# Kernel tuning notes

Measured on AMD Instinct MI355X. Metric: run time of the kernel, lower is better.

Reference implementation:

```python
import jax, jax.numpy as jnp
import numpy as np

N, E, F, ED, H, G = 100000, 400000, 143, 6, 128, 4096
NL = 3   # num_layers -> NL-1 atom GATConv layers
NT = 2   # num_timesteps


def leaky(v):
    return jnp.where(v >= 0, v, 0.01 * v)  # torch default negative_slope=0.01


def gru_cell(xin, hid, Wi, Wh, bi, bh):
    # torch.nn.GRUCell, gate order r,z,n
    gi = xin @ Wi.T + bi
    gh = hid @ Wh.T + bh
    ir, iz, inn = jnp.split(gi, 3, axis=-1)
    hr, hz, hn = jnp.split(gh, 3, axis=-1)
    r = jax.nn.sigmoid(ir + hr)
    z = jax.nn.sigmoid(iz + hz)
    n = jnp.tanh(inn + r * hn)
    return (1.0 - z) * n + z * hid


def seg_softmax(a, seg, num):
    m = jax.ops.segment_max(a, seg, num_segments=num)
    m = jnp.where(jnp.isfinite(m), m, 0.0)
    e = jnp.exp(a - m[seg])
    s = jax.ops.segment_sum(e, seg, num_segments=num)
    return e / (s[seg] + 1e-16)


def afp_forward(x, edge_attr, lin1_W, lin1_b, gc_lin1_W, gc_att_l, gc_att_r,
                gc_lin2_W, gc_bias, gru0_Wi, gru0_Wh, gru0_bi, gru0_bh,
                atom_W, atom_att_src, atom_att_dst, atom_bias,
                atom_gru_Wi, atom_gru_Wh, atom_gru_bi, atom_gru_bh,
                mol_W, mol_att_src, mol_att_dst, mol_bias,
                mol_gru_Wi, mol_gru_Wh, mol_gru_bi, mol_gru_bh,
                lin2_W, lin2_b, cls_W1, cls_b1, cls_W2, cls_b2,
                edge_index, batch, num_graphs):
    src, dst = edge_index[0], edge_index[1]
    Nn = x.shape[0]
    # lin1 + leaky_relu
    x0 = leaky(x @ lin1_W.T + lin1_b)                                  # [N,H]
    # GATEConv (edge-feature gated attention)
    t = leaky(jnp.concatenate([x0[src], edge_attr], axis=-1) @ gc_lin1_W.T)  # [E,H]
    alpha = leaky(t @ gc_att_l + (x0 @ gc_att_r)[dst])                 # [E]
    alpha = seg_softmax(alpha, dst, Nn)
    x2 = x0 @ gc_lin2_W.T
    agg = jax.ops.segment_sum(x2[src] * alpha[:, None], dst, num_segments=Nn) + gc_bias
    h = jax.nn.elu(agg)
    xh = jax.nn.relu(gru_cell(h, x0, gru0_Wi, gru0_Wh, gru0_bi, gru0_bh))
    # atom GATConv layers (single head, no self loops, slope 0.01)
    for l in range(atom_W.shape[0]):
        xl = xh @ atom_W[l].T                                          # [N,H]
        a = leaky((xl @ atom_att_src[l])[src] + (xl @ atom_att_dst[l])[dst])
        a = seg_softmax(a, dst, Nn)
        agg = jax.ops.segment_sum(xl[src] * a[:, None], dst, num_segments=Nn) + atom_bias[l]
        h = jax.nn.elu(agg)
        xh = jax.nn.relu(gru_cell(h, xh, atom_gru_Wi[l], atom_gru_Wh[l], atom_gru_bi[l], atom_gru_bh[l]))
    # molecule readout: bipartite GATConv node->graph + GRU, NT timesteps
    out = jax.nn.relu(jax.ops.segment_sum(xh, batch, num_segments=num_graphs))  # [G,H]
    xm = xh @ mol_W.T
    a_src = xm @ mol_att_src                                           # [N]
    for _ in range(NT):
        om = out @ mol_W.T
        a = leaky(a_src + (om @ mol_att_dst)[batch])
        a = seg_softmax(a, batch, num_graphs)
        agg = jax.ops.segment_sum(xm * a[:, None], batch, num_segments=num_graphs) + mol_bias
        h = jax.nn.elu(agg)
        out = jax.nn.relu(gru_cell(h, out, mol_gru_Wi, mol_gru_Wh, mol_gru_bi, mol_gru_bh))
    emb = out @ lin2_W.T + lin2_b                                      # [G,H]
    y = jax.nn.relu(emb @ cls_W1.T + cls_b1) @ cls_W2.T + cls_b2       # [G,1]
    return y[:, 0]


def setup_inputs():
    key = jax.random.key(0)
    ks = iter(jax.random.split(key, 64))
    def rn(shape, s=0.08):
        return jax.random.normal(next(ks), shape, dtype=jnp.float32) * s
    return dict(
        x=jax.random.normal(next(ks), (N, F), dtype=jnp.float32),
        edge_attr=jax.random.normal(next(ks), (E, ED), dtype=jnp.float32),
        lin1_W=rn((H, F)), lin1_b=rn((H,)),
        gc_lin1_W=rn((H, H + ED)), gc_att_l=rn((H,)), gc_att_r=rn((H,)),
        gc_lin2_W=rn((H, H)), gc_bias=rn((H,)),
        gru0_Wi=rn((3 * H, H)), gru0_Wh=rn((3 * H, H)), gru0_bi=rn((3 * H,)), gru0_bh=rn((3 * H,)),
        atom_W=rn((NL - 1, H, H)), atom_att_src=rn((NL - 1, H)), atom_att_dst=rn((NL - 1, H)), atom_bias=rn((NL - 1, H)),
        atom_gru_Wi=rn((NL - 1, 3 * H, H)), atom_gru_Wh=rn((NL - 1, 3 * H, H)),
        atom_gru_bi=rn((NL - 1, 3 * H)), atom_gru_bh=rn((NL - 1, 3 * H)),
        mol_W=rn((H, H)), mol_att_src=rn((H,)), mol_att_dst=rn((H,)), mol_bias=rn((H,)),
        mol_gru_Wi=rn((3 * H, H)), mol_gru_Wh=rn((3 * H, H)), mol_gru_bi=rn((3 * H,)), mol_gru_bh=rn((3 * H,)),
        lin2_W=rn((H, H)), lin2_b=rn((H,)),
        cls_W1=rn((64, H)), cls_b1=rn((64,)), cls_W2=rn((1, 64)), cls_b2=rn((1,)),
        edge_index=jax.random.randint(next(ks), (2, E), 0, N),
        batch=jnp.sort(jax.random.randint(next(ks), (N,), 0, G)),
        num_graphs=G,
    )


def reference(x, edge_attr, lin1_W, lin1_b, gc_lin1_W, gc_att_l, gc_att_r,
              gc_lin2_W, gc_bias, gru0_Wi, gru0_Wh, gru0_bi, gru0_bh,
              atom_W, atom_att_src, atom_att_dst, atom_bias,
              atom_gru_Wi, atom_gru_Wh, atom_gru_bi, atom_gru_bh,
              mol_W, mol_att_src, mol_att_dst, mol_bias,
              mol_gru_Wi, mol_gru_Wh, mol_gru_bi, mol_gru_bh,
              lin2_W, lin2_b, cls_W1, cls_b1, cls_W2, cls_b2,
              edge_index, batch, num_graphs):
    return afp_forward(x, edge_attr, lin1_W, lin1_b, gc_lin1_W, gc_att_l, gc_att_r,
                       gc_lin2_W, gc_bias, gru0_Wi, gru0_Wh, gru0_bi, gru0_bh,
                       atom_W, atom_att_src, atom_att_dst, atom_bias,
                       atom_gru_Wi, atom_gru_Wh, atom_gru_bi, atom_gru_bh,
                       mol_W, mol_att_src, mol_att_dst, mol_bias,
                       mol_gru_Wi, mol_gru_Wh, mol_gru_bi, mol_gru_bh,
                       lin2_W, lin2_b, cls_W1, cls_b1, cls_W2, cls_b2,
                       edge_index, batch, num_graphs)
```

## Files before the change

kernel.cpp:

```cpp
#include <hip/hip_runtime.h>

#define NND 100000
#define NED 400000
#define FEAT 143
#define FEATP 160
#define EDIM 6
#define H 128
#define NG 4096
#define NBS 391

typedef __attribute__((ext_vector_type(8))) short bf8;
typedef __attribute__((ext_vector_type(4))) float f4;

__device__ __forceinline__ float b2f(unsigned short u){
  unsigned int x = ((unsigned int)u) << 16;
  return __builtin_bit_cast(float, x);
}
__device__ __forceinline__ unsigned short f2b(float f){
  unsigned int u = __builtin_bit_cast(unsigned int, f);
  u = u + 0x7fffu + ((u >> 16) & 1u);
  return (unsigned short)(u >> 16);
}
__device__ __forceinline__ float lk(float v){ return v >= 0.f ? v : 0.01f*v; }
__device__ __forceinline__ float eluf(float v){ return v > 0.f ? v : __expf(v) - 1.f; }
__device__ __forceinline__ float sgm(float v){ return 1.f/(1.f + __expf(-v)); }
__device__ __forceinline__ float wsum(float v){
  #pragma unroll
  for(int o=32;o>0;o>>=1) v += __shfl_xor(v,o);
  return v;
}
__device__ __forceinline__ bf8 cvt8(const float* p){
  f4 a = *(const f4*)p;
  f4 b = *(const f4*)(p+4);
  bf8 t;
  t[0]=(short)f2b(a[0]); t[1]=(short)f2b(a[1]); t[2]=(short)f2b(a[2]); t[3]=(short)f2b(a[3]);
  t[4]=(short)f2b(b[0]); t[5]=(short)f2b(b[1]); t[6]=(short)f2b(b[2]); t[7]=(short)f2b(b[3]);
  return t;
}

__global__ __launch_bounds__(256) void k_wfrag(const float* __restrict__ src, int lds, int srcK,
                                               unsigned short* __restrict__ dst, int NT, int KB){
  int i = blockIdx.x*256 + threadIdx.x;
  int total = NT*KB*512;
  if (i >= total) return;
  int j = i & 7, lane = (i>>3) & 63, kb = (i>>9) % KB, nt = i/(KB*512);
  int n = nt*16 + (lane & 15), k = kb*32 + (lane>>4)*8 + j;
  dst[i] = (k < srcK) ? f2b(src[(size_t)n*lds + k]) : (unsigned short)0;
}

__global__ __launch_bounds__(256) void k_hist(const int* __restrict__ ei, int* __restrict__ deg){
  int e = blockIdx.x*256 + threadIdx.x;
  if (e < NED) atomicAdd(&deg[ei[NED + e]], 1);
}
__global__ __launch_bounds__(256) void k_scan1(const int* __restrict__ deg, int* __restrict__ off, int* __restrict__ bsum){
  __shared__ int s[256];
  int i = blockIdx.x*256 + threadIdx.x;
  int v = (i < NND) ? deg[i] : 0;
  s[threadIdx.x] = v; __syncthreads();
  for(int o=1;o<256;o<<=1){
    int t = 0; if (threadIdx.x >= o) t = s[threadIdx.x - o];
    __syncthreads(); s[threadIdx.x] += t; __syncthreads();
  }
  if (i < NND) off[i] = s[threadIdx.x] - v;
  if (threadIdx.x == 255) bsum[blockIdx.x] = s[255];
}
__global__ __launch_bounds__(512) void k_scan2(int* __restrict__ bsum){
  __shared__ int s[512];
  int t = threadIdx.x;
  int v = (t < NBS) ? bsum[t] : 0;
  s[t] = v; __syncthreads();
  for(int o=1;o<512;o<<=1){
    int x = 0; if (t >= o) x = s[t - o];
    __syncthreads(); s[t] += x; __syncthreads();
  }
  if (t < NBS) bsum[t] = s[t] - v;
  if (t == 511) bsum[NBS] = s[511];
}
__global__ __launch_bounds__(256) void k_scan3(int* __restrict__ off, const int* __restrict__ bsum, int* __restrict__ cursor){
  int i = blockIdx.x*256 + threadIdx.x;
  if (i < NND){
    int v = off[i] + bsum[blockIdx.x];
    off[i] = v; cursor[i] = v;
  }
  if (i == 0) off[NND] = bsum[NBS];
}
__global__ __launch_bounds__(256) void k_scatter(const int* __restrict__ ei, int* __restrict__ cursor, int* __restrict__ perm){
  int e = blockIdx.x*256 + threadIdx.x;
  if (e < NED){
    int p = atomicAdd(&cursor[ei[NED + e]], 1);
    perm[p] = e;
  }
}
__global__ __launch_bounds__(256) void k_gstart(const int* __restrict__ batch, int* __restrict__ goff){
  int i = blockIdx.x*256 + threadIdx.x;
  if (i >= NND) return;
  int bi = batch[i];
  int bp = (i > 0) ? batch[i-1] : -1;
  for(int g = bp+1; g <= bi; g++) goff[g] = i;
  if (i == NND-1) for(int g = bi+1; g <= NG; g++) goff[g] = NND;
}

__global__ __launch_bounds__(256) void k_padx(const float* __restrict__ x, unsigned short* __restrict__ xp){
  int r = blockIdx.x*4 + (threadIdx.x >> 6);
  int lane = threadIdx.x & 63;
  if (r >= NND) return;
  for(int i = lane; i < FEATP; i += 64)
    xp[(size_t)r*FEATP + i] = (i < FEAT) ? f2b(x[(size_t)r*FEAT + i]) : (unsigned short)0;
}

template<int KB, int RT, bool ABF16, bool BIAS, int ACT, bool OBF16, int DOT>
__global__ __launch_bounds__(256) void k_gemm(const void* __restrict__ Ap, int lda,
        const unsigned short* __restrict__ Wf,
        const float* __restrict__ bias, void* __restrict__ Cp, int M,
        const float* __restrict__ v1, const float* __restrict__ v2,
        float* __restrict__ o1, float* __restrict__ o2)
{
  int tid = threadIdx.x, wave = tid >> 6, lane = tid & 63;
  int m = lane & 15, quad = lane >> 4;
  int r0 = blockIdx.x * (16*RT);
  bf8 a[RT][KB];
  #pragma unroll
  for(int rt=0; rt<RT; rt++){
    int row = r0 + rt*16 + m;
    if (ABF16){
      const unsigned short* base = (const unsigned short*)Ap + (size_t)row*lda + quad*8;
      #pragma unroll
      for(int kb=0;kb<KB;kb++) a[rt][kb] = *(const bf8*)(base + kb*32);
    } else {
      const float* base = (const float*)Ap + (size_t)row*lda + quad*8;
      #pragma unroll
      for(int kb=0;kb<KB;kb++) a[rt][kb] = cvt8(base + kb*32);
    }
  }
  float d1[RT][4], d2[RT][4];
  if (DOT >= 1){
    #pragma unroll
    for(int rt=0;rt<RT;rt++)
      #pragma unroll
      for(int i=0;i<4;i++){ d1[rt][i] = 0.f; if (DOT==2) d2[rt][i] = 0.f; }
  }
  #pragma unroll
  for(int ct=0;ct<2;ct++){
    int nt = wave*2 + ct;
    int n = nt*16 + m;
    const bf8* wf = (const bf8*)Wf + (size_t)nt*KB*64;
    bf8 b[KB];
    #pragma unroll
    for(int kb=0;kb<KB;kb++) b[kb] = wf[kb*64 + lane];
    float bv = BIAS ? bias[n] : 0.f;
    float vv1 = (DOT>=1) ? v1[n] : 0.f;
    float vv2 = (DOT==2) ? v2[n] : 0.f;
    #pragma unroll
    for(int rt=0;rt<RT;rt++){
      f4 acc = {0.f,0.f,0.f,0.f};
      #pragma unroll
      for(int kb=0;kb<KB;kb++)
        acc = __builtin_amdgcn_mfma_f32_16x16x32_bf16(a[rt][kb], b[kb], acc, 0, 0, 0);
      #pragma unroll
      for(int i=0;i<4;i++){
        int row = r0 + rt*16 + quad*4 + i;
        float v = acc[i] + bv;
        if (ACT == 1) v = lk(v);
        if (DOT >= 1){ d1[rt][i] += v*vv1; if (DOT==2) d2[rt][i] += v*vv2; }
        if (row < M){
          if (OBF16) ((unsigned short*)Cp)[(size_t)row*H + n] = f2b(v);
          else       ((float*)Cp)[(size_t)row*H + n] = v;
        }
      }
    }
  }
  if (DOT >= 1){
    #pragma unroll
    for(int rt=0;rt<RT;rt++){
      #pragma unroll
      for(int i=0;i<4;i++){
        float dd = d1[rt][i];
        #pragma unroll
        for(int o=1;o<16;o<<=1) dd += __shfl_xor(dd, o);
        int row = r0 + rt*16 + quad*4 + i;
        if (m == 0 && row < M) atomicAdd(&o1[row], dd);
        if (DOT == 2){
          float ee = d2[rt][i];
          #pragma unroll
          for(int o=1;o<16;o<<=1) ee += __shfl_xor(ee, o);
          if (m == 0 && row < M) atomicAdd(&o2[row], ee);
        }
      }
    }
  }
}

__global__ __launch_bounds__(256) void k_gemm2(const float* __restrict__ A,
        const unsigned short* __restrict__ Wf1, const unsigned short* __restrict__ Wf2,
        unsigned short* __restrict__ ux, int M)
{
  int tid = threadIdx.x, wave = tid >> 6, lane = tid & 63;
  int m = lane & 15, quad = lane >> 4;
  int r0 = blockIdx.x * 64;
  bf8 a[4][4];
  #pragma unroll
  for(int rt=0; rt<4; rt++){
    const float* base = A + (size_t)(r0 + rt*16 + m)*H + quad*8;
    #pragma unroll
    for(int kb=0;kb<4;kb++) a[rt][kb] = cvt8(base + kb*32);
  }
  #pragma unroll
  for(int ws=0; ws<2; ws++){
    const unsigned short* Wf = ws ? Wf2 : Wf1;
    #pragma unroll
    for(int ct=0;ct<2;ct++){
      int nt = wave*2 + ct;
      int n = nt*16 + m;
      const bf8* wf = (const bf8*)Wf + (size_t)nt*256;
      bf8 b[4];
      #pragma unroll
      for(int kb=0;kb<4;kb++) b[kb] = wf[kb*64 + lane];
      int pos = (n>>3)*16 + ws*8 + (n&7);
      #pragma unroll
      for(int rt=0;rt<4;rt++){
        f4 acc = {0.f,0.f,0.f,0.f};
        #pragma unroll
        for(int kb=0;kb<4;kb++)
          acc = __builtin_amdgcn_mfma_f32_16x16x32_bf16(a[rt][kb], b[kb], acc, 0, 0, 0);
        #pragma unroll
        for(int i=0;i<4;i++){
          int row = r0 + rt*16 + quad*4 + i;
          if (row < M) ux[(size_t)row*256 + pos] = f2b(acc[i]);
        }
      }
    }
  }
}

__global__ __launch_bounds__(256) void k_gru(const float* __restrict__ Xin,
      const float* __restrict__ Hid, float* __restrict__ Out,
      const unsigned short* __restrict__ Wif, const unsigned short* __restrict__ Whf,
      const float* __restrict__ bi, const float* __restrict__ bh_)
{
  int tid = threadIdx.x, wave = tid >> 6, lane = tid & 63;
  int m = lane & 15, quad = lane >> 4;
  int r0 = blockIdx.x * 32;
  bf8 ax[2][4], ah[2][4];
  #pragma unroll
  for(int rt=0;rt<2;rt++){
    const float* xb = Xin + (size_t)(r0+rt*16+m)*H + quad*8;
    const float* hb = Hid + (size_t)(r0+rt*16+m)*H + quad*8;
    #pragma unroll
    for(int kb=0;kb<4;kb++){
      ax[rt][kb] = cvt8(xb + kb*32);
      ah[rt][kb] = cvt8(hb + kb*32);
    }
  }
  __syncthreads();
  f4 rg[2][2], ng[2][2];
  #pragma unroll
  for(int c=0;c<2;c++){
    int nt = wave*2 + c;
    const bf8* wi = (const bf8*)Wif + (size_t)nt*256;
    const bf8* wh = (const bf8*)Whf + (size_t)nt*256;
    int col = nt*16 + m;
    float bb = bi[col] + bh_[col];
    #pragma unroll
    for(int rt=0;rt<2;rt++){
      f4 acc = {0.f,0.f,0.f,0.f};
      #pragma unroll
      for(int kb=0;kb<4;kb++){
        acc = __builtin_amdgcn_mfma_f32_16x16x32_bf16(ax[rt][kb], wi[kb*64+lane], acc,0,0,0);
        acc = __builtin_amdgcn_mfma_f32_16x16x32_bf16(ah[rt][kb], wh[kb*64+lane], acc,0,0,0);
      }
      #pragma unroll
      for(int i=0;i<4;i++) rg[c][rt][i] = sgm(acc[i] + bb);
    }
  }
  #pragma unroll
  for(int c=0;c<2;c++){
    int nt = 16 + wave*2 + c;
    const bf8* wi = (const bf8*)Wif + (size_t)nt*256;
    const bf8* wh = (const bf8*)Whf + (size_t)nt*256;
    int col = (wave*2+c)*16 + m;
    float bin_ = bi[col+256], bhn_ = bh_[col+256];
    #pragma unroll
    for(int rt=0;rt<2;rt++){
      f4 a1 = {0.f,0.f,0.f,0.f}, a2 = {0.f,0.f,0.f,0.f};
      #pragma unroll
      for(int kb=0;kb<4;kb++){
        a1 = __builtin_amdgcn_mfma_f32_16x16x32_bf16(ax[rt][kb], wi[kb*64+lane], a1,0,0,0);
        a2 = __builtin_amdgcn_mfma_f32_16x16x32_bf16(ah[rt][kb], wh[kb*64+lane], a2,0,0,0);
      }
      #pragma unroll
      for(int i=0;i<4;i++)
        ng[c][rt][i] = tanhf(a1[i] + bin_ + rg[c][rt][i]*(a2[i] + bhn_));
    }
  }
  #pragma unroll
  for(int c=0;c<2;c++){
    int nt = 8 + wave*2 + c;
    const bf8* wi = (const bf8*)Wif + (size_t)nt*256;
    const bf8* wh = (const bf8*)Whf + (size_t)nt*256;
    int col = (wave*2+c)*16 + m;
    float bb = bi[col+128] + bh_[col+128];
    #pragma unroll
    for(int rt=0;rt<2;rt++){
      f4 acc = {0.f,0.f,0.f,0.f};
      #pragma unroll
      for(int kb=0;kb<4;kb++){
        acc = __builtin_amdgcn_mfma_f32_16x16x32_bf16(ax[rt][kb], wi[kb*64+lane], acc,0,0,0);
        acc = __builtin_amdgcn_mfma_f32_16x16x32_bf16(ah[rt][kb], wh[kb*64+lane], acc,0,0,0);
      }
      #pragma unroll
      for(int i=0;i<4;i++){
        float zg = sgm(acc[i] + bb);
        int row = r0 + rt*16 + quad*4 + i;
        float hv = Hid[(size_t)row*H + col];
        float o = (1.f - zg)*ng[c][rt][i] + zg*hv;
        Out[(size_t)row*H + col] = fmaxf(o, 0.f);
      }
    }
  }
}

__global__ __launch_bounds__(256, 4) void k_gate_agg(
   const int* __restrict__ ei, const float* __restrict__ eattr,
   const float* __restrict__ gcW, const float* __restrict__ attl,
   const float* __restrict__ r, const unsigned short* __restrict__ ux,
   const float* __restrict__ gbias,
   const int* __restrict__ off, const int* __restrict__ perm,
   float* __restrict__ hout)
{
  int tid = threadIdx.x;
  int wave = tid >> 6, lane = tid & 63;
  int grp = lane >> 4, sub = lane & 15;
  int n = blockIdx.x*4 + wave;
  if (n >= NND) return;
  int c0 = sub*8;
  float W1e[48];
  #pragma unroll
  for(int c=0;c<8;c++)
    #pragma unroll
    for(int j=0;j<EDIM;j++)
      W1e[c*EDIM+j] = gcW[(size_t)(c0+c)*(H+EDIM) + H + j];
  float attl8[8];
  #pragma unroll
  for(int c=0;c<8;c++) attl8[c] = attl[c0+c];
  int o0 = off[n], deg = off[n+1] - o0;
  float rn = r[n];
  float mx = -3.4e38f, S = 0.f;
  float acc[8] = {0,0,0,0,0,0,0,0};
  for(int base=0; base<deg; base+=64){
    int cnt = min(deg - base, 64);
    int s_l = 0;
    float ea_l[EDIM] = {0,0,0,0,0,0};
    if (lane < cnt){
      int e = perm[o0 + base + lane];
      s_l = ei[e];
      const float* ep = eattr + (size_t)e*EDIM;
      #pragma unroll
      for(int j=0;j<EDIM;j++) ea_l[j] = ep[j];
    }
    #pragma unroll 1
    for(int k=0;k<16;k++){
      int l = grp + k*4;
      if (l >= cnt) break;
      int s = __shfl(s_l, l);
      float ea[EDIM];
      #pragma unroll
      for(int j=0;j<EDIM;j++) ea[j] = __shfl(ea_l[j], l);
      const unsigned short* rowp = ux + (size_t)s*256 + sub*16;
      bf8 uv = *(const bf8*)rowp;
      bf8 xv = *(const bf8*)(rowp + 8);
      float p = 0.f;
      #pragma unroll
      for(int c=0;c<8;c++){
        float ve = 0.f;
        #pragma unroll
        for(int j=0;j<EDIM;j++) ve += ea[j] * W1e[c*EDIM + j];
        float t = lk(b2f((unsigned short)uv[c]) + ve);
        p += t * attl8[c];
      }
      #pragma unroll
      for(int o=1;o<16;o<<=1) p += __shfl_xor(p, o);
      float araw = lk(p + rn);
      float mnew = fmaxf(mx, araw);
      float sc = __expf(mx - mnew);
      float w  = __expf(araw - mnew);
      S = S*sc + w;
      #pragma unroll
      for(int c=0;c<8;c++) acc[c] = acc[c]*sc + w*b2f((unsigned short)xv[c]);
      mx = mnew;
    }
  }
  #pragma unroll
  for(int o=16;o<64;o<<=1){
    float mo = __shfl_xor(mx, o);
    float So = __shfl_xor(S, o);
    float mnew = fmaxf(mx, mo);
    float sa = __expf(mx - mnew), sb = __expf(mo - mnew);
    S = S*sa + So*sb;
    #pragma unroll
    for(int c=0;c<8;c++){
      float ao = __shfl_xor(acc[c], o);
      acc[c] = acc[c]*sa + ao*sb;
    }
    mx = mnew;
  }
  float inv = 1.f/(S + 1e-16f);
  if (grp == 0){
    #pragma unroll
    for(int c=0;c<8;c++)
      hout[(size_t)n*H + c0 + c] = eluf(acc[c]*inv + gbias[c0+c]);
  }
}

__global__ __launch_bounds__(256) void k_atom_agg(
    const int* __restrict__ ei, const float* __restrict__ s1, const float* __restrict__ s2,
    const unsigned short* __restrict__ xl, const float* __restrict__ abias,
    const int* __restrict__ off, const int* __restrict__ perm,
    float* __restrict__ hout)
{
  int tid = threadIdx.x, wave = tid >> 6, lane = tid & 63;
  int grp = lane >> 4, sub = lane & 15;
  int n = blockIdx.x*4 + wave;
  if (n >= NND) return;
  int o0 = off[n], deg = off[n+1] - o0;
  int c0 = sub*8;
  float s2n = s2[n];
  float mx = -3.4e38f, S = 0.f;
  float acc[8] = {0,0,0,0,0,0,0,0};
  for(int base=0; base<deg; base+=64){
    int cnt = min(deg - base, 64);
    int s_l = 0; float ar_l = 0.f;
    if (lane < cnt){ int e = perm[o0 + base + lane]; s_l = ei[e]; ar_l = lk(s1[s_l] + s2n); }
    #pragma unroll 1
    for(int k=0;k<16;k++){
      int l = grp + k*4;
      if (l >= cnt) break;
      int s = __shfl(s_l, l);
      float araw = __shfl(ar_l, l);
      bf8 xv = *(const bf8*)(xl + (size_t)s*H + c0);
      float mnew = fmaxf(mx, araw);
      float sc = __expf(mx - mnew);
      float w  = __expf(araw - mnew);
      S = S*sc + w;
      #pragma unroll
      for(int c=0;c<8;c++) acc[c] = acc[c]*sc + w*b2f((unsigned short)xv[c]);
      mx = mnew;
    }
  }
  #pragma unroll
  for(int o=16;o<64;o<<=1){
    float mo = __shfl_xor(mx, o);
    float So = __shfl_xor(S, o);
    float mnew = fmaxf(mx, mo);
    float sa = __expf(mx - mnew), sb = __expf(mo - mnew);
    S = S*sa + So*sb;
    #pragma unroll
    for(int c=0;c<8;c++){
      float ao = __shfl_xor(acc[c], o);
      acc[c] = acc[c]*sa + ao*sb;
    }
    mx = mnew;
  }
  float inv = 1.f/(S + 1e-16f);
  if (grp == 0){
    #pragma unroll
    for(int c=0;c<8;c++)
      hout[(size_t)n*H + c0 + c] = eluf(acc[c]*inv + abias[c0+c]);
  }
}

__global__ __launch_bounds__(256) void k_seg0(const float* __restrict__ xh, const int* __restrict__ goff,
                                              float* __restrict__ outg)
{
  int g = blockIdx.x*4 + (threadIdx.x >> 6);
  if (g >= NG) return;
  int lane = threadIdx.x & 63;
  int gs = goff[g], ge = goff[g+1];
  int h0 = lane*2;
  float a0 = 0.f, a1 = 0.f;
  for(int n=gs;n<ge;n++){
    const float* p = xh + (size_t)n*H + h0;
    a0 += p[0]; a1 += p[1];
  }
  outg[(size_t)g*H + h0]   = fmaxf(a0, 0.f);
  outg[(size_t)g*H + h0+1] = fmaxf(a1, 0.f);
}

__global__ __launch_bounds__(256) void k_mol_agg(const float* __restrict__ asrc, const float* __restrict__ d,
    const unsigned short* __restrict__ xm, const int* __restrict__ goff,
    const float* __restrict__ mbias, float* __restrict__ hmol)
{
  int tid = threadIdx.x, wave = tid >> 6, lane = tid & 63;
  int grp = lane >> 4, sub = lane & 15;
  int g = blockIdx.x*4 + wave;
  if (g >= NG) return;
  int gs = goff[g], num = goff[g+1] - gs;
  int c0 = sub*8;
  float dg = d[g];
  float mx = -3.4e38f, S = 0.f;
  float acc[8] = {0,0,0,0,0,0,0,0};
  for(int base=0; base<num; base+=64){
    int cnt = min(num - base, 64);
    float ar_l = 0.f;
    if (lane < cnt) ar_l = lk(asrc[gs + base + lane] + dg);
    #pragma unroll 1
    for(int k=0;k<16;k++){
      int l = grp + k*4;
      if (l >= cnt) break;
      float araw = __shfl(ar_l, l);
      int node = gs + base + l;
      bf8 xv = *(const bf8*)(xm + (size_t)node*H + c0);
      float mnew = fmaxf(mx, araw);
      float sc = __expf(mx - mnew);
      float w  = __expf(araw - mnew);
      S = S*sc + w;
      #pragma unroll
      for(int c=0;c<8;c++) acc[c] = acc[c]*sc + w*b2f((unsigned short)xv[c]);
      mx = mnew;
    }
  }
  #pragma unroll
  for(int o=16;o<64;o<<=1){
    float mo = __shfl_xor(mx, o);
    float So = __shfl_xor(S, o);
    float mnew = fmaxf(mx, mo);
    float sa = __expf(mx - mnew), sb = __expf(mo - mnew);
    S = S*sa + So*sb;
    #pragma unroll
    for(int c=0;c<8;c++){
      float ao = __shfl_xor(acc[c], o);
      acc[c] = acc[c]*sa + ao*sb;
    }
    mx = mnew;
  }
  float inv = 1.f/(S + 1e-16f);
  if (grp == 0){
    #pragma unroll
    for(int c=0;c<8;c++)
      hmol[(size_t)g*H + c0 + c] = eluf(acc[c]*inv + mbias[c0+c]);
  }
}

__global__ __launch_bounds__(256) void k_cls(const float* __restrict__ emb,
   const float* __restrict__ W1, const float* __restrict__ b1,
   const float* __restrict__ W2, const float* __restrict__ b2,
   float* __restrict__ outp)
{
  __shared__ float W1t[H*64];
  int tid = threadIdx.x;
  for(int i=tid;i<64*H;i+=256){
    int l = i >> 7, hh = i & 127;
    W1t[hh*64 + l] = W1[i];
  }
  __syncthreads();
  int wave = tid >> 6, lane = tid & 63;
  int g = blockIdx.x*4 + wave;
  if (g >= NG) return;
  const float* er = emb + (size_t)g*H;
  float acc = 0.f;
  for(int hh=0;hh<H;hh++) acc += er[hh] * W1t[hh*64 + lane];
  float hid = fmaxf(acc + b1[lane], 0.f);
  float p = hid * W2[lane];
  p = wsum(p);
  if (lane == 0) outp[g] = p + b2[0];
}

extern "C" void kernel_launch(void* const* d_in, const int* in_sizes, int n_in,
                              void* d_out, int out_size, void* d_ws, size_t ws_size,
                              hipStream_t stream)
{
  const float* x      = (const float*)d_in[0];
  const float* eattr  = (const float*)d_in[1];
  const float* lin1W  = (const float*)d_in[2];
  const float* lin1b  = (const float*)d_in[3];
  const float* gcW    = (const float*)d_in[4];
  const float* gcatl  = (const float*)d_in[5];
  const float* gcatr  = (const float*)d_in[6];
  const float* gcW2   = (const float*)d_in[7];
  const float* gcb    = (const float*)d_in[8];
  const float* g0Wi   = (const float*)d_in[9];
  const float* g0Wh   = (const float*)d_in[10];
  const float* g0bi   = (const float*)d_in[11];
  const float* g0bh   = (const float*)d_in[12];
  const float* aW     = (const float*)d_in[13];
  const float* aas    = (const float*)d_in[14];
  const float* aad    = (const float*)d_in[15];
  const float* ab     = (const float*)d_in[16];
  const float* agWi   = (const float*)d_in[17];
  const float* agWh   = (const float*)d_in[18];
  const float* agbi   = (const float*)d_in[19];
  const float* agbh   = (const float*)d_in[20];
  const float* mW     = (const float*)d_in[21];
  const float* mas    = (const float*)d_in[22];
  const float* mad    = (const float*)d_in[23];
  const float* mb     = (const float*)d_in[24];
  const float* mgWi   = (const float*)d_in[25];
  const float* mgWh   = (const float*)d_in[26];
  const float* mgbi   = (const float*)d_in[27];
  const float* mgbh   = (const float*)d_in[28];
  const float* l2W    = (const float*)d_in[29];
  const float* l2b    = (const float*)d_in[30];
  const float* cW1    = (const float*)d_in[31];
  const float* cb1    = (const float*)d_in[32];
  const float* cW2    = (const float*)d_in[33];
  const float* cb2    = (const float*)d_in[34];
  const int* ei    = (const int*)d_in[35];
  const int* batch = (const int*)d_in[36];
  float* outp = (float*)d_out;

  char* p = (char*)d_ws;
  auto alloc = [&](size_t sz)->void*{ void* q = (void*)p; p += (sz + 511) & ~(size_t)511; return q; };
  float* x0            = (float*)alloc((size_t)NND*H*4);
  unsigned short* ux   = (unsigned short*)alloc((size_t)NND*256*2);
  unsigned short* bu   = (unsigned short*)alloc((size_t)NND*H*2);
  float* xh            = (float*)alloc((size_t)NND*H*4);
  float* bh            = (float*)alloc((size_t)NND*H*4);
  unsigned short* xm   = (unsigned short*)x0;
  unsigned short* xp   = (unsigned short*)bh;
  char* z0 = p;
  float* rbuf          = (float*)alloc((size_t)NND*4);
  float* s1a           = (float*)alloc((size_t)NND*4);
  float* s2a           = (float*)alloc((size_t)NND*4);
  float* s1b           = (float*)alloc((size_t)NND*4);
  float* s2b           = (float*)alloc((size_t)NND*4);
  float* asrc          = (float*)alloc((size_t)NND*4);
  float* dg0           = (float*)alloc((size_t)NG*4);
  float* dg1           = (float*)alloc((size_t)NG*4);
  size_t zbytes = (size_t)(p - z0);
  int* deg             = (int*)alloc((size_t)NND*4);
  int* off             = (int*)alloc((size_t)(NND+1)*4);
  int* cursor          = (int*)alloc((size_t)NND*4);
  int* perm            = (int*)alloc((size_t)NED*4);
  int* bsum            = (int*)alloc((size_t)(NBS+1)*4);
  int* goff            = (int*)alloc((size_t)(NG+1)*4);
  float* outg          = (float*)alloc((size_t)NG*H*4);
  float* hmol          = (float*)alloc((size_t)NG*H*4);
  float* om            = (float*)alloc((size_t)NG*H*4);
  float* emb           = (float*)alloc((size_t)NG*H*4);
  unsigned short* wp     = (unsigned short*)alloc((size_t)8*5*512*2);
  unsigned short* gcWnb  = (unsigned short*)alloc((size_t)H*H*2);
  unsigned short* gcW2b  = (unsigned short*)alloc((size_t)H*H*2);
  unsigned short* g0Wib  = (unsigned short*)alloc((size_t)3*H*H*2);
  unsigned short* g0Whb  = (unsigned short*)alloc((size_t)3*H*H*2);
  unsigned short* aWb    = (unsigned short*)alloc((size_t)2*H*H*2);
  unsigned short* agWib  = (unsigned short*)alloc((size_t)2*3*H*H*2);
  unsigned short* agWhb  = (unsigned short*)alloc((size_t)2*3*H*H*2);
  unsigned short* mWb    = (unsigned short*)alloc((size_t)H*H*2);
  unsigned short* l2Wb   = (unsigned short*)alloc((size_t)H*H*2);
  unsigned short* mgWib  = (unsigned short*)alloc((size_t)3*H*H*2);
  unsigned short* mgWhb  = (unsigned short*)alloc((size_t)3*H*H*2);

  const int HH = H*H, H3H = 3*H*H;
  k_wfrag<<<80 ,256,0,stream>>>(lin1W, FEAT, FEAT, wp, 8, 5);
  k_wfrag<<<64 ,256,0,stream>>>(gcW, H+EDIM, H, gcWnb, 8, 4);
  k_wfrag<<<64 ,256,0,stream>>>(gcW2, H, H, gcW2b, 8, 4);
  k_wfrag<<<192,256,0,stream>>>(g0Wi, H, H, g0Wib, 24, 4);
  k_wfrag<<<192,256,0,stream>>>(g0Wh, H, H, g0Whb, 24, 4);
  for(int l=0;l<2;l++){
    k_wfrag<<<64 ,256,0,stream>>>(aW + (size_t)l*HH, H, H, aWb + (size_t)l*HH, 8, 4);
    k_wfrag<<<192,256,0,stream>>>(agWi + (size_t)l*H3H, H, H, agWib + (size_t)l*H3H, 24, 4);
    k_wfrag<<<192,256,0,stream>>>(agWh + (size_t)l*H3H, H, H, agWhb + (size_t)l*H3H, 24, 4);
  }
  k_wfrag<<<64 ,256,0,stream>>>(mW, H, H, mWb, 8, 4);
  k_wfrag<<<64 ,256,0,stream>>>(l2W, H, H, l2Wb, 8, 4);
  k_wfrag<<<192,256,0,stream>>>(mgWi, H, H, mgWib, 24, 4);
  k_wfrag<<<192,256,0,stream>>>(mgWh, H, H, mgWhb, 24, 4);

  hipMemsetAsync(z0, 0, zbytes, stream);
  hipMemsetAsync(deg, 0, (size_t)NND*4, stream);
  k_hist<<<1563,256,0,stream>>>(ei, deg);
  k_scan1<<<NBS,256,0,stream>>>(deg, off, bsum);
  k_scan2<<<1,512,0,stream>>>(bsum);
  k_scan3<<<NBS,256,0,stream>>>(off, bsum, cursor);
  k_scatter<<<1563,256,0,stream>>>(ei, cursor, perm);
  k_gstart<<<NBS,256,0,stream>>>(batch, goff);

  const int GB = (NND + 63)/64;
  k_padx<<<25000,256,0,stream>>>(x, xp);
  k_gemm<5,4,true,true,1,false,1><<<GB,256,0,stream>>>(xp, FEATP, wp, lin1b, x0, NND,
                                                       gcatr, nullptr, rbuf, nullptr);
  k_gemm2<<<GB,256,0,stream>>>(x0, gcWnb, gcW2b, ux, NND);
  k_gate_agg<<<25000,256,0,stream>>>(ei, eattr, gcW, gcatl, rbuf, ux, gcb, off, perm, bh);
  k_gru<<<NND/32,256,0,stream>>>(bh, x0, xh, g0Wib, g0Whb, g0bi, g0bh);

  float* s1l[2] = {s1a, s1b};
  float* s2l[2] = {s2a, s2b};
  for(int l=0;l<2;l++){
    k_gemm<4,4,false,false,0,true,2><<<GB,256,0,stream>>>(xh, H, aWb + (size_t)l*HH, nullptr, bu, NND,
                                                          aas + l*H, aad + l*H, s1l[l], s2l[l]);
    k_atom_agg<<<25000,256,0,stream>>>(ei, s1l[l], s2l[l], bu, ab + l*H, off, perm, bh);
    k_gru<<<NND/32,256,0,stream>>>(bh, xh, xh, agWib + (size_t)l*H3H, agWhb + (size_t)l*H3H,
                                   agbi + l*3*H, agbh + l*3*H);
  }

  k_seg0<<<NG/4,256,0,stream>>>(xh, goff, outg);
  k_gemm<4,4,false,false,0,true,1><<<GB,256,0,stream>>>(xh, H, mWb, nullptr, xm, NND,
                                                        mas, nullptr, asrc, nullptr);
  float* dgt[2] = {dg0, dg1};
  for(int t=0;t<2;t++){
    k_gemm<4,4,false,false,0,false,1><<<(NG+63)/64,256,0,stream>>>(outg, H, mWb, nullptr, om, NG,
                                                                   mad, nullptr, dgt[t], nullptr);
    k_mol_agg<<<NG/4,256,0,stream>>>(asrc, dgt[t], xm, goff, mb, hmol);
    k_gru<<<NG/32,256,0,stream>>>(hmol, outg, outg, mgWib, mgWhb, mgbi, mgbh);
  }

  k_gemm<4,4,false,true,0,false,0><<<(NG+63)/64,256,0,stream>>>(outg, H, l2Wb, l2b, emb, NG,
                                                                nullptr, nullptr, nullptr, nullptr);
  k_cls<<<NG/4,256,0,stream>>>(emb, cW1, cb1, cW2, cb2, outp);
}
```

Before: 1.092 ms.

## Pre-sort edge sources and attributes by destination, batch weight conversions into one launch

The CSR scatter now writes source indices and edge attributes directly in destination-sorted order. The gate and atom aggregation kernels can then read them contiguously instead of going through the perm indirection and gathering from random edge positions. All 17 weight-fragment conversion launches are merged into a single kernel driven by a descriptor struct. The deg memset is folded into the existing zero-fill region. The scatter kernel does more scattered writes and uses extra memory for the sorted attribute copy.

```diff
diff --git a/kernel.cpp b/kernel.cpp
--- a/kernel.cpp
+++ b/kernel.cpp
@@ -38,14 +38,19 @@
   return t;
 }
 
-__global__ __launch_bounds__(256) void k_wfrag(const float* __restrict__ src, int lds, int srcK,
-                                               unsigned short* __restrict__ dst, int NT, int KB){
-  int i = blockIdx.x*256 + threadIdx.x;
-  int total = NT*KB*512;
+struct WDesc { const float* src; unsigned short* dst; int lds, srcK, NT, KB; };
+struct WPack { WDesc d[17]; int nd; };
+#define WBLK 192
+__global__ __launch_bounds__(256) void k_wfrag_all(WPack P){
+  int di = blockIdx.x / WBLK;
+  if (di >= P.nd) return;
+  WDesc w = P.d[di];
+  int total = w.NT*w.KB*512;
+  int i = (blockIdx.x % WBLK)*256 + threadIdx.x;
   if (i >= total) return;
-  int j = i & 7, lane = (i>>3) & 63, kb = (i>>9) % KB, nt = i/(KB*512);
+  int j = i & 7, lane = (i>>3) & 63, kb = (i>>9) % w.KB, nt = i/(w.KB*512);
   int n = nt*16 + (lane & 15), k = kb*32 + (lane>>4)*8 + j;
-  dst[i] = (k < srcK) ? f2b(src[(size_t)n*lds + k]) : (unsigned short)0;
+  w.dst[i] = (k < w.srcK) ? f2b(w.src[(size_t)n*w.lds + k]) : (unsigned short)0;
 }
 
 __global__ __launch_bounds__(256) void k_hist(const int* __restrict__ ei, int* __restrict__ deg){
@@ -84,11 +89,17 @@
   }
   if (i == 0) off[NND] = bsum[NBS];
 }
-__global__ __launch_bounds__(256) void k_scatter(const int* __restrict__ ei, int* __restrict__ cursor, int* __restrict__ perm){
+__global__ __launch_bounds__(256) void k_scatter(const int* __restrict__ ei, const float* __restrict__ eattr,
+                                                 int* __restrict__ cursor,
+                                                 int* __restrict__ srcs, float* __restrict__ ea_srt){
   int e = blockIdx.x*256 + threadIdx.x;
   if (e < NED){
     int p = atomicAdd(&cursor[ei[NED + e]], 1);
-    perm[p] = e;
+    srcs[p] = ei[e];
+    const float* ep = eattr + (size_t)e*EDIM;
+    float* dp = ea_srt + (size_t)p*EDIM;
+    #pragma unroll
+    for(int j=0;j<EDIM;j++) dp[j] = ep[j];
   }
 }
 __global__ __launch_bounds__(256) void k_gstart(const int* __restrict__ batch, int* __restrict__ goff){
@@ -320,11 +331,10 @@
 }
 
 __global__ __launch_bounds__(256, 4) void k_gate_agg(
-   const int* __restrict__ ei, const float* __restrict__ eattr,
    const float* __restrict__ gcW, const float* __restrict__ attl,
    const float* __restrict__ r, const unsigned short* __restrict__ ux,
    const float* __restrict__ gbias,
-   const int* __restrict__ off, const int* __restrict__ perm,
+   const int* __restrict__ off, const int* __restrict__ srcs, const float* __restrict__ ea_srt,
    float* __restrict__ hout)
 {
   int tid = threadIdx.x;
@@ -351,9 +361,9 @@
     int s_l = 0;
     float ea_l[EDIM] = {0,0,0,0,0,0};
     if (lane < cnt){
-      int e = perm[o0 + base + lane];
-      s_l = ei[e];
-      const float* ep = eattr + (size_t)e*EDIM;
+      int idx = o0 + base + lane;
+      s_l = srcs[idx];
+      const float* ep = ea_srt + (size_t)idx*EDIM;
       #pragma unroll
       for(int j=0;j<EDIM;j++) ea_l[j] = ep[j];
     }
@@ -412,9 +422,9 @@
 }
 
 __global__ __launch_bounds__(256) void k_atom_agg(
-    const int* __restrict__ ei, const float* __restrict__ s1, const float* __restrict__ s2,
+    const float* __restrict__ s1, const float* __restrict__ s2,
     const unsigned short* __restrict__ xl, const float* __restrict__ abias,
-    const int* __restrict__ off, const int* __restrict__ perm,
+    const int* __restrict__ off, const int* __restrict__ srcs,
     float* __restrict__ hout)
 {
   int tid = threadIdx.x, wave = tid >> 6, lane = tid & 63;
@@ -429,7 +439,7 @@
   for(int base=0; base<deg; base+=64){
     int cnt = min(deg - base, 64);
     int s_l = 0; float ar_l = 0.f;
-    if (lane < cnt){ int e = perm[o0 + base + lane]; s_l = ei[e]; ar_l = lk(s1[s_l] + s2n); }
+    if (lane < cnt){ s_l = srcs[o0 + base + lane]; ar_l = lk(s1[s_l] + s2n); }
     #pragma unroll 1
     for(int k=0;k<16;k++){
       int l = grp + k*4;
@@ -625,11 +635,12 @@
   float* asrc          = (float*)alloc((size_t)NND*4);
   float* dg0           = (float*)alloc((size_t)NG*4);
   float* dg1           = (float*)alloc((size_t)NG*4);
+  int* deg             = (int*)alloc((size_t)NND*4);
   size_t zbytes = (size_t)(p - z0);
-  int* deg             = (int*)alloc((size_t)NND*4);
   int* off             = (int*)alloc((size_t)(NND+1)*4);
   int* cursor          = (int*)alloc((size_t)NND*4);
-  int* perm            = (int*)alloc((size_t)NED*4);
+  int* srcs            = (int*)alloc((size_t)NED*4);
+  float* ea_srt        = (float*)alloc((size_t)NED*EDIM*4);
   int* bsum            = (int*)alloc((size_t)(NBS+1)*4);
   int* goff            = (int*)alloc((size_t)(NG+1)*4);
   float* outg          = (float*)alloc((size_t)NG*H*4);
@@ -650,28 +661,34 @@
   unsigned short* mgWhb  = (unsigned short*)alloc((size_t)3*H*H*2);
 
   const int HH = H*H, H3H = 3*H*H;
-  k_wfrag<<<80 ,256,0,stream>>>(lin1W, FEAT, FEAT, wp, 8, 5);
-  k_wfrag<<<64 ,256,0,stream>>>(gcW, H+EDIM, H, gcWnb, 8, 4);
-  k_wfrag<<<64 ,256,0,stream>>>(gcW2, H, H, gcW2b, 8, 4);
-  k_wfrag<<<192,256,0,stream>>>(g0Wi, H, H, g0Wib, 24, 4);
-  k_wfrag<<<192,256,0,stream>>>(g0Wh, H, H, g0Whb, 24, 4);
+  WPack wpk;
+  int nd = 0;
+  auto addw = [&](const float* s, unsigned short* d, int lds, int srcK, int NT, int KB){
+    wpk.d[nd++] = WDesc{s, d, lds, srcK, NT, KB};
+  };
+  addw(lin1W, wp, FEAT, FEAT, 8, 5);
+  addw(gcW, gcWnb, H+EDIM, H, 8, 4);
+  addw(gcW2, gcW2b, H, H, 8, 4);
+  addw(g0Wi, g0Wib, H, H, 24, 4);
+  addw(g0Wh, g0Whb, H, H, 24, 4);
   for(int l=0;l<2;l++){
-    k_wfrag<<<64 ,256,0,stream>>>(aW + (size_t)l*HH, H, H, aWb + (size_t)l*HH, 8, 4);
-    k_wfrag<<<192,256,0,stream>>>(agWi + (size_t)l*H3H, H, H, agWib + (size_t)l*H3H, 24, 4);
-    k_wfrag<<<192,256,0,stream>>>(agWh + (size_t)l*H3H, H, H, agWhb + (size_t)l*H3H, 24, 4);
-  }
-  k_wfrag<<<64 ,256,0,stream>>>(mW, H, H, mWb, 8, 4);
-  k_wfrag<<<64 ,256,0,stream>>>(l2W, H, H, l2Wb, 8, 4);
-  k_wfrag<<<192,256,0,stream>>>(mgWi, H, H, mgWib, 24, 4);
-  k_wfrag<<<192,256,0,stream>>>(mgWh, H, H, mgWhb, 24, 4);
+    addw(aW + (size_t)l*HH, aWb + (size_t)l*HH, H, H, 8, 4);
+    addw(agWi + (size_t)l*H3H, agWib + (size_t)l*H3H, H, H, 24, 4);
+    addw(agWh + (size_t)l*H3H, agWhb + (size_t)l*H3H, H, H, 24, 4);
+  }
+  addw(mW, mWb, H, H, 8, 4);
+  addw(l2W, l2Wb, H, H, 8, 4);
+  addw(mgWi, mgWib, H, H, 24, 4);
+  addw(mgWh, mgWhb, H, H, 24, 4);
+  wpk.nd = nd;
+  k_wfrag_all<<<nd*WBLK,256,0,stream>>>(wpk);
 
   hipMemsetAsync(z0, 0, zbytes, stream);
-  hipMemsetAsync(deg, 0, (size_t)NND*4, stream);
   k_hist<<<1563,256,0,stream>>>(ei, deg);
   k_scan1<<<NBS,256,0,stream>>>(deg, off, bsum);
   k_scan2<<<1,512,0,stream>>>(bsum);
   k_scan3<<<NBS,256,0,stream>>>(off, bsum, cursor);
-  k_scatter<<<1563,256,0,stream>>>(ei, cursor, perm);
+  k_scatter<<<1563,256,0,stream>>>(ei, eattr, cursor, srcs, ea_srt);
   k_gstart<<<NBS,256,0,stream>>>(batch, goff);
 
   const int GB = (NND + 63)/64;
@@ -679,7 +696,7 @@
   k_gemm<5,4,true,true,1,false,1><<<GB,256,0,stream>>>(xp, FEATP, wp, lin1b, x0, NND,
                                                        gcatr, nullptr, rbuf, nullptr);
   k_gemm2<<<GB,256,0,stream>>>(x0, gcWnb, gcW2b, ux, NND);
-  k_gate_agg<<<25000,256,0,stream>>>(ei, eattr, gcW, gcatl, rbuf, ux, gcb, off, perm, bh);
+  k_gate_agg<<<25000,256,0,stream>>>(gcW, gcatl, rbuf, ux, gcb, off, srcs, ea_srt, bh);
   k_gru<<<NND/32,256,0,stream>>>(bh, x0, xh, g0Wib, g0Whb, g0bi, g0bh);
 
   float* s1l[2] = {s1a, s1b};
@@ -687,7 +704,7 @@
   for(int l=0;l<2;l++){
     k_gemm<4,4,false,false,0,true,2><<<GB,256,0,stream>>>(xh, H, aWb + (size_t)l*HH, nullptr, bu, NND,
                                                           aas + l*H, aad + l*H, s1l[l], s2l[l]);
-    k_atom_agg<<<25000,256,0,stream>>>(ei, s1l[l], s2l[l], bu, ab + l*H, off, perm, bh);
+    k_atom_agg<<<25000,256,0,stream>>>(s1l[l], s2l[l], bu, ab + l*H, off, srcs, bh);
     k_gru<<<NND/32,256,0,stream>>>(bh, xh, xh, agWib + (size_t)l*H3H, agWhb + (size_t)l*H3H,
                                    agbi + l*3*H, agbh + l*3*H);
   }
```

Result: faster. 1.057 ms (-3.2%).
